# Performance work log

Hardware: AMD Instinct MI355X
Metric: run time of the kernel (lower is better)

The kernel has to match this reference:

```python
import jax, jax.numpy as jnp
import numpy as np
from jax import lax

# pywt Wavelet('db4') decomposition filters
DEC_LO = jnp.array([-0.010597401784997278, 0.032883011666982945, 0.030841381835986965,
                    -0.18703481171888114, -0.02798376941698385, 0.6308807679295904,
                    0.7148465705525415, 0.23037781330885523], dtype=jnp.float32)
DEC_HI = jnp.array([-0.23037781330885523, 0.7148465705525415, -0.6308807679295904,
                    -0.02798376941698385, 0.18703481171888114, 0.030841381835986965,
                    -0.032883011666982945, -0.010597401784997278], dtype=jnp.float32)


def dwt_level(x, lo, hi):
    # single-level pywt dwt, mode='symmetric', along last axis
    f = lo.shape[0]
    p = f - 1
    pad = [(0, 0)] * (x.ndim - 1) + [(p, p)]
    xe = jnp.pad(x, pad, mode='symmetric')[..., 1:]  # offset 1 matches pywt phase
    lead = x.shape[:-1]
    xin = xe.reshape(-1, 1, xe.shape[-1])            # [N,1,L]
    filt = jnp.stack([lo[::-1], hi[::-1]])[:, None, :]  # flip: true convolution, [2,1,f]
    out = lax.conv_general_dilated(xin, filt, (2,), 'VALID')  # [N,2,floor((n+f-1)/2)]
    cA = out[:, 0].reshape(lead + (-1,))
    cD = out[:, 1].reshape(lead + (-1,))
    return cA, cD


def wavedec4(x):
    # pywt.wavedec(x,'db4',level=4) concatenated: [cA4,cD4,cD3,cD2,cD1]
    details = []
    a = x
    for _ in range(4):
        a, d = dwt_level(a, DEC_LO, DEC_HI)
        details.append(d)
    return jnp.concatenate([a] + details[::-1], axis=-1)


def lstm_last(xs, w_ih, w_hh, b_ih, b_hh):
    # torch LSTM (gate order i,f,g,o); returns last timestep hidden state
    B, T, _ = xs.shape
    H = w_hh.shape[1]
    h0 = jnp.zeros((B, H), xs.dtype)
    c0 = jnp.zeros((B, H), xs.dtype)
    b = b_ih + b_hh

    def step(carry, x_t):
        h, c = carry
        gates = x_t @ w_ih.T + h @ w_hh.T + b
        i, f, g, o = jnp.split(gates, 4, axis=-1)
        c = jax.nn.sigmoid(f) * c + jax.nn.sigmoid(i) * jnp.tanh(g)
        h = jax.nn.sigmoid(o) * jnp.tanh(c)
        return (h, c), None

    (h, _), _ = lax.scan(step, (h0, c0), jnp.swapaxes(xs, 0, 1))
    return h


def setup_inputs() -> dict:
    key = jax.random.key(0)
    ks = jax.random.split(key, 9)
    B, S, T = 256, 1024, 21
    return {
        'x': jax.random.normal(ks[0], (B, S, T), jnp.float32),
        'conv_w': jax.random.normal(ks[1], (64, 78, 3), jnp.float32) * 0.06,
        'conv_b': jax.random.normal(ks[2], (64,), jnp.float32) * 0.06,
        'w_ih': jax.random.normal(ks[3], (128, 64), jnp.float32) * 0.12,
        'w_hh': jax.random.normal(ks[4], (128, 32), jnp.float32) * 0.17,
        'b_ih': jax.random.normal(ks[5], (128,), jnp.float32) * 0.17,
        'b_hh': jax.random.normal(ks[6], (128,), jnp.float32) * 0.17,
        'fc_w': jax.random.normal(ks[7], (1, 32), jnp.float32) * 0.17,
        'fc_b': jax.random.normal(ks[8], (1,), jnp.float32) * 0.17,
    }


def reference(x, conv_w, conv_b, w_ih, w_hh, b_ih, b_hh, fc_w, fc_b):
    freq = jnp.abs(jnp.fft.rfft(x, axis=2))          # [B,S,11]
    tf = wavedec4(x)                                 # [B,S,46]
    combined = jnp.concatenate([x, freq, tf], axis=2)  # [B,S,78]
    combined = jnp.swapaxes(combined, 1, 2)          # [B,78,S]
    y = lax.conv_general_dilated(combined, conv_w, (1,), [(1, 1)]) + conv_b[None, :, None]
    y = jax.nn.relu(y)
    B, C, S = y.shape
    y = y.reshape(B, C, S // 2, 2).max(axis=-1)      # max_pool1d(k=2,s=2)
    y = jnp.transpose(y, (0, 2, 1))                  # [B,S//2,64]
    h = lstm_last(y, w_ih, w_hh, b_ih, b_hh)         # [B,32]
    return h @ fc_w.T + fc_b                         # [B,1]
```

## Files before the change

kernel.cpp:

```cpp
#include <hip/hip_runtime.h>
#include <math.h>

typedef _Float16 half8 __attribute__((ext_vector_type(8)));
typedef float floatx16 __attribute__((ext_vector_type(16)));
typedef float float2v __attribute__((ext_vector_type(2)));

constexpr float L2E = 1.4426950408889634f;

constexpr float DLO[8] = {-0.010597401784997278f, 0.032883011666982945f, 0.030841381835986965f,
                          -0.18703481171888114f, -0.02798376941698385f, 0.6308807679295904f,
                          0.7148465705525415f, 0.23037781330885523f};
constexpr float DHI[8] = {-0.23037781330885523f, 0.7148465705525415f, -0.6308807679295904f,
                          -0.02798376941698385f, 0.18703481171888114f, 0.030841381835986965f,
                          -0.032883011666982945f, -0.010597401784997278f};

constexpr float CT21[21] = {
  1.0f,          0.95557281f,  0.82623877f,  0.62348980f,  0.36534102f,  0.07473009f,
  -0.22252093f, -0.5f,        -0.73305187f, -0.90096887f, -0.98883083f,
  -0.98883083f, -0.90096887f, -0.73305187f, -0.5f,        -0.22252093f,
  0.07473009f,   0.36534102f,  0.62348980f,  0.82623877f,  0.95557281f};
constexpr float ST21[21] = {
  0.0f,          0.29475517f,  0.56332006f,  0.78183148f,  0.93087375f,  0.99720380f,
  0.97492791f,   0.86602540f,  0.68017274f,  0.43388374f,  0.14904227f,
  -0.14904227f, -0.43388374f, -0.68017274f, -0.86602540f, -0.97492791f,
  -0.99720380f, -0.93087375f, -0.78183148f, -0.56332006f, -0.29475517f};

template<int N>
__device__ __forceinline__ void dwt_step(const float* in, float* a, float* d) {
  constexpr int NO = (N + 7) / 2;
#pragma unroll
  for (int i = 0; i < NO; i++) {
    float sa = 0.f, sd = 0.f;
#pragma unroll
    for (int j = 0; j < 8; j++) {
      int rel = 2 * i + j - 6;
      int idx = (rel < 0) ? (-rel - 1) : ((rel >= N) ? (2 * N - rel - 1) : rel);
      float v = in[idx];
      sa = fmaf(v, DLO[7 - j], sa);
      sd = fmaf(v, DHI[7 - j], sd);
    }
    a[i] = sa;
    d[i] = sd;
  }
}

__device__ __forceinline__ void gload_lds16(const void* g, void* l) {
  __builtin_amdgcn_global_load_lds(
      (const __attribute__((address_space(1))) unsigned int*)g,
      (__attribute__((address_space(3))) unsigned int*)l, 16, 0, 0);
}

__device__ __forceinline__ void feature_row(const float* __restrict__ xr,
                                            _Float16* hrow) {
  float xx[21];
#pragma unroll
  for (int t = 0; t < 21; t++) xx[t] = xr[t];

#pragma unroll
  for (int i = 78; i < 88; i++) hrow[i] = (_Float16)0.f;

#pragma unroll
  for (int t = 0; t < 21; t++) hrow[t] = (_Float16)xx[t];

#pragma unroll
  for (int k = 0; k < 11; k++) {
    float re = 0.f, im = 0.f;
#pragma unroll
    for (int t = 0; t < 21; t++) {
      const int m = (k * t) % 21;
      re = fmaf(xx[t], CT21[m], re);
      im = fmaf(xx[t], ST21[m], im);
    }
    hrow[21 + k] = (_Float16)sqrtf(re * re + im * im);
  }

  float a1[14], d1[14];
  dwt_step<21>(xx, a1, d1);
#pragma unroll
  for (int i = 0; i < 14; i++) hrow[64 + i] = (_Float16)d1[i];
  float a2[10], d2[10];
  dwt_step<14>(a1, a2, d2);
#pragma unroll
  for (int i = 0; i < 10; i++) hrow[54 + i] = (_Float16)d2[i];
  float a3[8], d3[8];
  dwt_step<10>(a2, a3, d3);
#pragma unroll
  for (int i = 0; i < 8; i++) hrow[46 + i] = (_Float16)d3[i];
  float a4[7], d4[7];
  dwt_step<8>(a3, a4, d4);
#pragma unroll
  for (int i = 0; i < 7; i++) {
    hrow[32 + i] = (_Float16)a4[i];
    hrow[39 + i] = (_Float16)d4[i];
  }
}

__global__ __launch_bounds__(256) void wprep_kernel(const float* __restrict__ cw,
                                                    const float* __restrict__ w_ih,
                                                    const float* __restrict__ b_ih,
                                                    const float* __restrict__ b_hh,
                                                    _Float16* __restrict__ WbT,
                                                    _Float16* __restrict__ wih16,
                                                    float* __restrict__ biasI) {
  int idx = blockIdx.x * 256 + threadIdx.x;
  if (idx < 64 * 264) {
    int o = idx / 264, k = idx - o * 264;
    float v = 0.f;
    if (k < 240) {
      int dk = k / 80, c = k - dk * 80;
      if (c < 78) v = cw[o * 234 + c * 3 + dk];
    }
    WbT[idx] = (_Float16)v;
  } else if (idx < 16896 + 8192) {
    int j = idx - 16896;
    wih16[j] = (_Float16)(L2E * w_ih[j]);
  } else if (idx < 16896 + 8192 + 128) {
    int g = idx - 16896 - 8192;
    int p = ((g & 63) << 1) | (g >> 6);
    biasI[p] = L2E * (b_ih[g] + b_hh[g]);
  }
}

__device__ __forceinline__ float bcast_lane(float v, int k) {
  return __uint_as_float(__builtin_amdgcn_readlane(__float_as_uint(v), k));
}

#if __has_builtin(__builtin_amdgcn_exp2f)
#define EXP2F __builtin_amdgcn_exp2f
#else
#define EXP2F exp2f
#endif

#if __has_builtin(__builtin_amdgcn_permlane32_swap)
__device__ __forceinline__ float swap_half(float x) {
  auto r = __builtin_amdgcn_permlane32_swap(__float_as_uint(x), __float_as_uint(x),
                                            false, false);
  return __uint_as_float(r[1]);
}
#else
__device__ __forceinline__ float swap_half(float x) { return __shfl_down(x, 32); }
#endif

__device__ __forceinline__ void lstm_step(float& h, float& c, float2v xg,
                                          const float* __restrict__ wA,
                                          const float* __restrict__ wB, bool lo) {
  float hs[32];
#pragma unroll
  for (int k = 0; k < 32; k++) hs[k] = bcast_lane(h, k);

  float aA0 = xg.x, aA1 = 0.f, aB0 = xg.y, aB1 = 0.f;
#pragma unroll
  for (int k = 0; k < 32; k += 2) {
    aA0 = fmaf(hs[k], wA[k], aA0);
    aB0 = fmaf(hs[k], wB[k], aB0);
    aA1 = fmaf(hs[k + 1], wA[k + 1], aA1);
    aB1 = fmaf(hs[k + 1], wB[k + 1], aB1);
  }
  const float gA = aA0 + aA1;
  const float gB = aB0 + aB1;

  float sA = __builtin_amdgcn_rcpf(1.0f + EXP2F(-gA));

  float argB = lo ? (gB + gB) : (-gB);
  float rB = __builtin_amdgcn_rcpf(EXP2F(argB) + 1.0f);
  float sB = lo ? fmaf(-2.f, rB, 1.f) : rB;

  float fv = swap_half(sA);
  float ov = swap_half(sB);
  c = fmaf(fv, c, sA * sB);
  float rc = __builtin_amdgcn_rcpf(EXP2F(c * (2.f * L2E)) + 1.0f);
  float ov2 = ov + ov;
  h = fmaf(-ov2, rc, ov);
}

__device__ __forceinline__ void prod_barrier(int* pb, int& target) {
  target += 3;
  __builtin_amdgcn_s_waitcnt(0);
  if ((threadIdx.x & 63) == 0)
    __hip_atomic_fetch_add(pb, 1, __ATOMIC_RELEASE, __HIP_MEMORY_SCOPE_WORKGROUP);
  while (__hip_atomic_load(pb, __ATOMIC_ACQUIRE, __HIP_MEMORY_SCOPE_WORKGROUP) < target) {
  }
}

__global__ __launch_bounds__(256, 1)
__attribute__((amdgpu_waves_per_eu(1, 1)))
void fused_kernel(const float* __restrict__ x,
                  const _Float16* __restrict__ WbT,
                  const float* __restrict__ cbias,
                  const _Float16* __restrict__ wih16,
                  const float* __restrict__ biasI,
                  const float* __restrict__ w_hh,
                  const float* __restrict__ fc_w,
                  const float* __restrict__ fc_b,
                  float* __restrict__ Xp,
                  float* __restrict__ out) {
  __shared__ __align__(16) char smem[61184];
  __shared__ int ready;
  __shared__ int pbar;
  _Float16* At = (_Float16*)smem;
  _Float16* Bt = (_Float16*)(smem + 24576);
  _Float16* yt = (_Float16*)smem;
  _Float16* wl = (_Float16*)(smem + 9216);
  float* biasl = (float*)(smem + 27648);
  float* Xpt   = (float*)(smem + 28160);
  float* bl    = (float*)(smem + 60928);

  const int tid = threadIdx.x;
  const int b = blockIdx.x;

  if (tid == 0) { ready = 0; pbar = 0; }
  if (tid < 64) bl[tid] = cbias[tid];
  __syncthreads();

  if (tid < 64) {
    const int L = tid;
    const bool lo = (L < 32);
    float wA[32], wB[32];
    {
      const float4* rA = (const float4*)(w_hh + L * 32);
      const float4* rB = (const float4*)(w_hh + (L + 64) * 32);
#pragma unroll
      for (int q = 0; q < 8; q++) {
        float4 a4 = rA[q], b4 = rB[q];
        wA[4 * q + 0] = L2E * a4.x; wA[4 * q + 1] = L2E * a4.y;
        wA[4 * q + 2] = L2E * a4.z; wA[4 * q + 3] = L2E * a4.w;
        wB[4 * q + 0] = L2E * b4.x; wB[4 * q + 1] = L2E * b4.y;
        wB[4 * q + 2] = L2E * b4.z; wB[4 * q + 3] = L2E * b4.w;
      }
    }

    float h = 0.f, c = 0.f;
    for (int k = 0; k < 8; k++) {
      while (__hip_atomic_load(&ready, __ATOMIC_ACQUIRE, __HIP_MEMORY_SCOPE_WORKGROUP) < k + 1)
        __builtin_amdgcn_s_sleep(2);
      const float* xp = Xp + ((size_t)b * 512 + (size_t)k * 64) * 128;
      float2v p2[4];
#pragma unroll
      for (int u = 0; u < 4; u++) p2[u] = *(const float2v*)&xp[u * 128 + 2 * L];
      for (int t0 = 0; t0 < 64; t0 += 4) {
        float2v c2[4];
#pragma unroll
        for (int u = 0; u < 4; u++) c2[u] = p2[u];
        if (t0 + 4 < 64) {
#pragma unroll
          for (int u = 0; u < 4; u++)
            p2[u] = *(const float2v*)&xp[(t0 + 4 + u) * 128 + 2 * L];
        }
#pragma unroll
        for (int u = 0; u < 4; u++) lstm_step(h, c, c2[u], wA, wB, lo);
      }
    }

    float v = lo ? h * fc_w[L & 31] : 0.f;
#pragma unroll
    for (int off = 32; off > 0; off >>= 1) v += __shfl_down(v, off);
    if (L == 0) out[b] = v + fc_b[0];
  } else {
    const int ptid = tid - 64;
    const int pw = (tid >> 6) - 1;
    const int lane = tid & 63, ml = lane & 31, kg = lane >> 5;
    int bt = 0;

    for (int k = 0; k < 8; k++) {
      const int s0 = k * 128;

      {
        const char* srcB = (const char*)WbT;
#pragma unroll
        for (int j = 0; j < 11; j++) {
          const int idx = j * 192 + ptid;
          gload_lds16(srcB + (size_t)idx * 16, (char*)Bt + (size_t)idx * 16);
        }
      }
      if (ptid < 130) {
        const int s = s0 - 1 + ptid;
        __align__(16) _Float16 hrow[88];
        if (s < 0 || s > 1023) {
#pragma unroll
          for (int i = 0; i < 88; i++) hrow[i] = (_Float16)0.f;
        } else {
          feature_row(x + ((size_t)(b << 10) + s) * 21, hrow);
        }
        uint4* dst = (uint4*)&At[ptid * 88];
        const uint4* src = (const uint4*)hrow;
#pragma unroll
        for (int i = 0; i < 11; i++) dst[i] = src[i];
      }
      prod_barrier(&pbar, bt);

      float pooled[3][8];
      {
        int cc = 0;
        for (int wt = pw; wt < 8; wt += 3, cc++) {
          const int mt = wt & 3, nt = wt >> 2;
          floatx16 acc = {};
#pragma unroll
          for (int ks = 0; ks < 15; ks++) {
            const int kb = ks * 16 + kg * 8;
            const int dk = (kb >= 160) ? 2 : ((kb >= 80) ? 1 : 0);
            const int cofs = kb - dk * 80;
            half8 av = *(const half8*)&At[(mt * 32 + ml + dk) * 88 + cofs];
            half8 bv = *(const half8*)&Bt[(nt * 32 + ml) * 264 + kb];
            acc = __builtin_amdgcn_mfma_f32_32x32x16_f16(av, bv, acc, 0, 0, 0);
          }
          const float bo = bl[nt * 32 + ml];
#pragma unroll
          for (int p = 0; p < 8; p++)
            pooled[cc][p] = fmaxf(fmaxf(acc[2 * p], acc[2 * p + 1]) + bo, 0.f);
        }
      }
      prod_barrier(&pbar, bt);

      {
        int cc = 0;
        for (int wt = pw; wt < 8; wt += 3, cc++) {
          const int mt = wt & 3, nt = wt >> 2;
#pragma unroll
          for (int p = 0; p < 8; p++) {
            const int toff = (p & 1) + ((p >> 1) << 2);
            const int t = mt * 16 + (kg << 1) + toff;
            yt[t * 72 + nt * 32 + ml] = (_Float16)pooled[cc][p];
          }
        }
        for (int i = ptid; i < 2048; i += 192) {
          int g = i >> 4, c4 = i & 15;
          *(uint2*)(wl + g * 72 + c4 * 4) = *(const uint2*)(wih16 + g * 64 + c4 * 4);
        }
        if (ptid < 128) biasl[ptid] = biasI[ptid];
      }
      prod_barrier(&pbar, bt);

      for (int wt = pw; wt < 8; wt += 3) {
        const int pm = wt & 1, pn = wt >> 1;
        floatx16 pa = {};
#pragma unroll
        for (int kq = 0; kq < 4; kq++) {
          const int k0 = kq * 16 + kg * 8;
          half8 av = *(const half8*)&yt[(pm * 32 + ml) * 72 + k0];
          half8 bv = *(const half8*)&wl[(pn * 32 + ml) * 72 + k0];
          pa = __builtin_amdgcn_mfma_f32_32x32x16_f16(av, bv, pa, 0, 0, 0);
        }
        const int gi = pn * 32 + ml;
        const int pp = ((gi & 63) << 1) | (gi >> 6);
#pragma unroll
        for (int reg = 0; reg < 16; reg++) {
          const int row = (reg & 3) + 8 * (reg >> 2) + 4 * kg;
          Xpt[(pm * 32 + row) * 128 + pp] = pa[reg];
        }
      }
      prod_barrier(&pbar, bt);

      {
        float* xpg = Xp + ((size_t)b * 512 + (size_t)k * 64) * 128;
        for (int i = ptid; i < 2048; i += 192) {
          const int r = i >> 5, c4 = (i & 31) << 2;
          float4 v = *(float4*)&Xpt[r * 128 + c4];
          float4 bb = *(float4*)&biasl[c4];
          v.x += bb.x; v.y += bb.y; v.z += bb.z; v.w += bb.w;
          *(float4*)&xpg[r * 128 + c4] = v;
        }
      }
      prod_barrier(&pbar, bt);

      if (tid == 64)
        __hip_atomic_fetch_add(&ready, 1, __ATOMIC_RELEASE, __HIP_MEMORY_SCOPE_WORKGROUP);
    }
  }
}

extern "C" void kernel_launch(void* const* d_in, const int* in_sizes, int n_in,
                              void* d_out, int out_size, void* d_ws, size_t ws_size,
                              hipStream_t stream) {
  const float* x      = (const float*)d_in[0];
  const float* conv_w = (const float*)d_in[1];
  const float* conv_b = (const float*)d_in[2];
  const float* w_ih   = (const float*)d_in[3];
  const float* w_hh   = (const float*)d_in[4];
  const float* b_ih   = (const float*)d_in[5];
  const float* b_hh   = (const float*)d_in[6];
  const float* fc_w   = (const float*)d_in[7];
  const float* fc_b   = (const float*)d_in[8];
  float* out = (float*)d_out;

  char* wsb = (char*)d_ws;
  float*    Xp    = (float*)wsb;
  _Float16* WbT   = (_Float16*)(wsb + 67108864);
  _Float16* wih16 = (_Float16*)(wsb + 67108864 + 33792);
  float*    biasI = (float*)(wsb + 67108864 + 33792 + 16384);

  wprep_kernel<<<dim3(99), dim3(256), 0, stream>>>(conv_w, w_ih, b_ih, b_hh,
                                                   WbT, wih16, biasI);
  fused_kernel<<<dim3(256), dim3(256), 0, stream>>>(x, WbT, conv_b, wih16, biasI,
                                                    w_hh, fc_w, fc_b, Xp, out);
}
```

Before: 198.1 us.

## Move LSTM recurrent matvec onto MFMA with split-fp16 hidden state

Replaces the per-lane scalar FMA recurrent matvec, which used 32 readlane broadcasts per step, with 16x16x32 fp16 MFMAs. The hidden state is split into high and low fp16 parts to keep accuracy, and is redistributed with DPP swaps and ds_bpermute. The gate-input layout in Xp and biasI is re-permuted so each lane reads 8 contiguous gate values, and each lane now owns two hidden units. This removes the serial scalar dependency chain but adds 16 dependent MFMAs plus permute latency on every timestep, which could make the serial recurrence slower.

```diff
diff --git a/kernel.cpp b/kernel.cpp
--- a/kernel.cpp
+++ b/kernel.cpp
@@ -2,8 +2,10 @@
 #include <math.h>
 
 typedef _Float16 half8 __attribute__((ext_vector_type(8)));
+typedef _Float16 half2v __attribute__((ext_vector_type(2)));
 typedef float floatx16 __attribute__((ext_vector_type(16)));
-typedef float float2v __attribute__((ext_vector_type(2)));
+typedef float floatx4 __attribute__((ext_vector_type(4)));
+typedef int int4v __attribute__((ext_vector_type(4)));
 
 constexpr float L2E = 1.4426950408889634f;
 
@@ -116,13 +118,9 @@
     wih16[j] = (_Float16)(L2E * w_ih[j]);
   } else if (idx < 16896 + 8192 + 128) {
     int g = idx - 16896 - 8192;
-    int p = ((g & 63) << 1) | (g >> 6);
+    int p = ((g & 15) << 3) | (g >> 4);
     biasI[p] = L2E * (b_ih[g] + b_hh[g]);
   }
-}
-
-__device__ __forceinline__ float bcast_lane(float v, int k) {
-  return __uint_as_float(__builtin_amdgcn_readlane(__float_as_uint(v), k));
 }
 
 #if __has_builtin(__builtin_amdgcn_exp2f)
@@ -131,46 +129,67 @@
 #define EXP2F exp2f
 #endif
 
-#if __has_builtin(__builtin_amdgcn_permlane32_swap)
-__device__ __forceinline__ float swap_half(float x) {
-  auto r = __builtin_amdgcn_permlane32_swap(__float_as_uint(x), __float_as_uint(x),
-                                            false, false);
-  return __uint_as_float(r[1]);
-}
-#else
-__device__ __forceinline__ float swap_half(float x) { return __shfl_down(x, 32); }
-#endif
-
-__device__ __forceinline__ void lstm_step(float& h, float& c, float2v xg,
-                                          const float* __restrict__ wA,
-                                          const float* __restrict__ wB, bool lo) {
-  float hs[32];
-#pragma unroll
-  for (int k = 0; k < 32; k++) hs[k] = bcast_lane(h, k);
-
-  float aA0 = xg.x, aA1 = 0.f, aB0 = xg.y, aB1 = 0.f;
-#pragma unroll
-  for (int k = 0; k < 32; k += 2) {
-    aA0 = fmaf(hs[k], wA[k], aA0);
-    aB0 = fmaf(hs[k], wB[k], aB0);
-    aA1 = fmaf(hs[k + 1], wA[k + 1], aA1);
-    aB1 = fmaf(hs[k + 1], wB[k + 1], aB1);
-  }
-  const float gA = aA0 + aA1;
-  const float gB = aB0 + aB1;
-
-  float sA = __builtin_amdgcn_rcpf(1.0f + EXP2F(-gA));
-
-  float argB = lo ? (gB + gB) : (-gB);
-  float rB = __builtin_amdgcn_rcpf(EXP2F(argB) + 1.0f);
-  float sB = lo ? fmaf(-2.f, rB, 1.f) : rB;
-
-  float fv = swap_half(sA);
-  float ov = swap_half(sB);
-  c = fmaf(fv, c, sA * sB);
-  float rc = __builtin_amdgcn_rcpf(EXP2F(c * (2.f * L2E)) + 1.0f);
-  float ov2 = ov + ov;
-  h = fmaf(-ov2, rc, ov);
+__device__ __forceinline__ float dpp_swap1(float x) {
+  int r = __builtin_amdgcn_update_dpp(0, __builtin_bit_cast(int, x),
+                                      0xB1, 0xF, 0xF, true);
+  return __builtin_bit_cast(float, r);
+}
+
+__device__ __forceinline__ int pkrtz_i(float a, float b) {
+  auto h = __builtin_amdgcn_cvt_pkrtz(a, b);
+  return __builtin_bit_cast(int, h);
+}
+
+__device__ __forceinline__ float sigm2(float g) {
+  return __builtin_amdgcn_rcpf(1.0f + EXP2F(-g));
+}
+__device__ __forceinline__ float tanh2(float g) {
+  return fmaf(-2.f, __builtin_amdgcn_rcpf(EXP2F(g + g) + 1.0f), 1.f);
+}
+
+__device__ __forceinline__ void lstm_step_mfma(
+    float& h0, float& h1, float& c0, float& c1,
+    const half8* __restrict__ wf, const int4v bpa, bool selhi,
+    float4 xpa, float4 xpb) {
+  int q0 = pkrtz_i(h0, dpp_swap1(h0));
+  int q1 = pkrtz_i(h1, dpp_swap1(h1));
+  int S = selhi ? q1 : q0;
+  float hh0 = (float)__builtin_bit_cast(half2v, q0).x;
+  float hh1 = (float)__builtin_bit_cast(half2v, q1).x;
+  float l0 = h0 - hh0, l1 = h1 - hh1;
+  int r0 = pkrtz_i(l0, dpp_swap1(l0));
+  int r1 = pkrtz_i(l1, dpp_swap1(l1));
+  int Sl = selhi ? r1 : r0;
+
+  int4v Ai, Li;
+#pragma unroll
+  for (int i = 0; i < 4; i++) {
+    Ai[i] = __builtin_amdgcn_ds_bpermute(bpa[i], S);
+    Li[i] = __builtin_amdgcn_ds_bpermute(bpa[i], Sl);
+  }
+  half8 Ah = __builtin_bit_cast(half8, Ai);
+  half8 Al = __builtin_bit_cast(half8, Li);
+
+  float xg[8] = {xpa.x, xpa.y, xpa.z, xpa.w, xpb.x, xpb.y, xpb.z, xpb.w};
+  float g8[8];
+#pragma unroll
+  for (int g = 0; g < 8; g++) {
+    floatx4 ci = {xg[g], 0.f, 0.f, 0.f};
+    floatx4 t0 = __builtin_amdgcn_mfma_f32_16x16x32_f16(Ah, wf[g], ci, 0, 0, 0);
+    floatx4 t1 = __builtin_amdgcn_mfma_f32_16x16x32_f16(Al, wf[g], t0, 0, 0, 0);
+    g8[g] = t1[0];
+  }
+
+  float si0 = sigm2(g8[0]), si1 = sigm2(g8[1]);
+  float sf0 = sigm2(g8[2]), sf1 = sigm2(g8[3]);
+  float tg0 = tanh2(g8[4]), tg1 = tanh2(g8[5]);
+  float so0 = sigm2(g8[6]), so1 = sigm2(g8[7]);
+  c0 = fmaf(sf0, c0, si0 * tg0);
+  c1 = fmaf(sf1, c1, si1 * tg1);
+  float rc0 = __builtin_amdgcn_rcpf(EXP2F(c0 * (2.0f * L2E)) + 1.0f);
+  float rc1 = __builtin_amdgcn_rcpf(EXP2F(c1 * (2.0f * L2E)) + 1.0f);
+  h0 = fmaf(-(so0 + so0), rc0, so0);
+  h1 = fmaf(-(so1 + so1), rc1, so1);
 }
 
 __device__ __forceinline__ void prod_barrier(int* pb, int& target) {
@@ -213,48 +232,59 @@
   __syncthreads();
 
   if (tid < 64) {
-    const int L = tid;
-    const bool lo = (L < 32);
-    float wA[32], wB[32];
-    {
-      const float4* rA = (const float4*)(w_hh + L * 32);
-      const float4* rB = (const float4*)(w_hh + (L + 64) * 32);
-#pragma unroll
-      for (int q = 0; q < 8; q++) {
-        float4 a4 = rA[q], b4 = rB[q];
-        wA[4 * q + 0] = L2E * a4.x; wA[4 * q + 1] = L2E * a4.y;
-        wA[4 * q + 2] = L2E * a4.z; wA[4 * q + 3] = L2E * a4.w;
-        wB[4 * q + 0] = L2E * b4.x; wB[4 * q + 1] = L2E * b4.y;
-        wB[4 * q + 2] = L2E * b4.z; wB[4 * q + 3] = L2E * b4.w;
-      }
-    }
-
-    float h = 0.f, c = 0.f;
+    const int col = tid & 15, grp = tid >> 4;
+    const bool selhi = (tid & 16) != 0;
+
+    half8 wf[8];
+#pragma unroll
+    for (int g = 0; g < 8; g++) {
+      const float* wr = w_hh + (g * 16 + col) * 32 + grp * 8;
+      float4 wa = *(const float4*)wr;
+      float4 wb = *(const float4*)(wr + 4);
+      half8 v;
+      v[0] = (_Float16)(L2E * wa.x); v[1] = (_Float16)(L2E * wa.y);
+      v[2] = (_Float16)(L2E * wa.z); v[3] = (_Float16)(L2E * wa.w);
+      v[4] = (_Float16)(L2E * wb.x); v[5] = (_Float16)(L2E * wb.y);
+      v[6] = (_Float16)(L2E * wb.z); v[7] = (_Float16)(L2E * wb.w);
+      wf[g] = v;
+    }
+
+    int4v bpa;
+#pragma unroll
+    for (int i = 0; i < 4; i++) {
+      const int src = (grp < 2) ? (8 * grp + 2 * i) : (16 + 8 * (grp - 2) + 2 * i);
+      bpa[i] = src * 4;
+    }
+
+    float h0 = 0.f, h1 = 0.f, c0 = 0.f, c1 = 0.f;
     for (int k = 0; k < 8; k++) {
       while (__hip_atomic_load(&ready, __ATOMIC_ACQUIRE, __HIP_MEMORY_SCOPE_WORKGROUP) < k + 1)
         __builtin_amdgcn_s_sleep(2);
-      const float* xp = Xp + ((size_t)b * 512 + (size_t)k * 64) * 128;
-      float2v p2[4];
-#pragma unroll
-      for (int u = 0; u < 4; u++) p2[u] = *(const float2v*)&xp[u * 128 + 2 * L];
-      for (int t0 = 0; t0 < 64; t0 += 4) {
-        float2v c2[4];
-#pragma unroll
-        for (int u = 0; u < 4; u++) c2[u] = p2[u];
-        if (t0 + 4 < 64) {
-#pragma unroll
-          for (int u = 0; u < 4; u++)
-            p2[u] = *(const float2v*)&xp[(t0 + 4 + u) * 128 + 2 * L];
-        }
-#pragma unroll
-        for (int u = 0; u < 4; u++) lstm_step(h, c, c2[u], wA, wB, lo);
-      }
-    }
-
-    float v = lo ? h * fc_w[L & 31] : 0.f;
-#pragma unroll
-    for (int off = 32; off > 0; off >>= 1) v += __shfl_down(v, off);
-    if (L == 0) out[b] = v + fc_b[0];
+      const float* xp = Xp + ((size_t)b * 512 + (size_t)k * 64) * 128 + col * 8;
+      float4 xa0 = *(const float4*)xp;
+      float4 xa1 = *(const float4*)(xp + 4);
+      float4 xb0 = *(const float4*)(xp + 128);
+      float4 xb1 = *(const float4*)(xp + 132);
+      for (int t = 0; t < 64; t += 2) {
+        lstm_step_mfma(h0, h1, c0, c1, wf, bpa, selhi, xa0, xa1);
+        if (t < 62) {
+          xa0 = *(const float4*)(xp + (t + 2) * 128);
+          xa1 = *(const float4*)(xp + (t + 2) * 128 + 4);
+        }
+        lstm_step_mfma(h0, h1, c0, c1, wf, bpa, selhi, xb0, xb1);
+        if (t < 62) {
+          xb0 = *(const float4*)(xp + (t + 3) * 128);
+          xb1 = *(const float4*)(xp + (t + 3) * 128 + 4);
+        }
+      }
+    }
+
+    float v = h0 * fc_w[col] + h1 * fc_w[col + 16];
+    v += __shfl_down(v, 8);
+    v += __shfl_down(v, 4);
+    v += __shfl_down(v, 2);
+    v += __shfl_down(v, 1);
+    if (tid == 0) out[b] = v + fc_b[0];
   } else {
     const int ptid = tid - 64;
     const int pw = (tid >> 6) - 1;
@@ -341,7 +371,7 @@
           pa = __builtin_amdgcn_mfma_f32_32x32x16_f16(av, bv, pa, 0, 0, 0);
         }
         const int gi = pn * 32 + ml;
-        const int pp = ((gi & 63) << 1) | (gi >> 6);
+        const int pp = ((gi & 15) << 3) | (gi >> 4);
 #pragma unroll
         for (int reg = 0; reg < 16; reg++) {
           const int row = (reg & 3) + 8 * (reg >> 2) + 4 * kg;
```

New measurement: 295.2 us. 49.0% more time.
